# Kernel tuning notes

Hardware: AMD Instinct MI355X
Metric: run time of the kernel (lower is better)

## Reference

```python
import jax, jax.numpy as jnp
import numpy as np

B, T, C = 2, 4096, 768
H = 12
D = C // H  # head_dim = 64
SCALE = np.sqrt(D).astype(np.float32)


def setup_inputs() -> dict:
    key = jax.random.key(0)
    ks = jax.random.split(key, 5)
    s = 0.02
    return {
        "x": jax.random.normal(ks[0], (B, T, C), dtype=jnp.float32),
        "Wqkv": jax.random.normal(ks[1], (C, 3 * C), dtype=jnp.float32) * s,
        "bqkv": jnp.zeros((3 * C,), dtype=jnp.float32),
        "Wout": jax.random.normal(ks[2], (C, C), dtype=jnp.float32) * s,
        "bout": jnp.zeros((C,), dtype=jnp.float32),
    }


def reference(x, Wqkv, bqkv, Wout, bout):
    Bx, Tx, Cx = x.shape
    qkv = x @ Wqkv + bqkv                                   # [B,T,3C]
    qkv = qkv.reshape(Bx, Tx, 3, H, D)
    q, k, v = [jnp.moveaxis(qkv[:, :, i], 2, 1) for i in range(3)]  # each [B,H,T,D]
    attn = jnp.einsum("bhqd,bhkd->bhqk", q, k) / SCALE      # [B,H,T,T]
    causal = jnp.tril(jnp.ones((Tx, Tx), dtype=bool))
    attn = jnp.where(causal, attn, jnp.float32(-jnp.inf))
    attn = jax.nn.softmax(attn, axis=-1)
    out = jnp.einsum("bhqk,bhkd->bhqd", attn, v)            # [B,H,T,D]
    out = jnp.moveaxis(out, 1, 2).reshape(Bx, Tx, Cx)       # [B,T,C]
    return out @ Wout + bout
```

## Files before the change

kernel.cpp:

```cpp
#include <hip/hip_runtime.h>
#include <hip/hip_bf16.h>

#define T_DIM 4096
#define H_N 12
#define D_H 64
#define C_DIM 768
#define B_N 2

typedef short bf16x8 __attribute__((ext_vector_type(8)));
typedef float f32x4 __attribute__((ext_vector_type(4)));
typedef float f32x16 __attribute__((ext_vector_type(16)));

__device__ __forceinline__ short f2bf(float f) {
    union { float f; unsigned u; } x; x.f = f;
    unsigned r = x.u + 0x7fffu + ((x.u >> 16) & 1u);
    return (short)(r >> 16);
}
__device__ __forceinline__ unsigned pk2bf(float a, float b) {
    union { float f; unsigned u; } x, y; x.f = a; y.f = b;
    unsigned ua = x.u + 0x7fffu + ((x.u >> 16) & 1u);
    unsigned ub = y.u + 0x7fffu + ((y.u >> 16) & 1u);
    return (ua >> 16) | (ub & 0xffff0000u);
}
__device__ __forceinline__ unsigned pktrunc(float lo, float hi) {
    union { float f; unsigned u; } a, b; a.f = lo; b.f = hi;
    return __builtin_amdgcn_perm(b.u, a.u, 0x07060302u);
}
__device__ __forceinline__ float bf2f(short s) {
    union { unsigned u; float f; } x; x.u = ((unsigned)(unsigned short)s) << 16;
    return x.f;
}

__device__ __forceinline__ void async_copy16(const void* g, void* l) {
    __builtin_amdgcn_global_load_lds(
        (const __attribute__((address_space(1))) unsigned*)g,
        (__attribute__((address_space(3))) unsigned*)l, 16, 0, 0);
}

#define Q_SCALE 0.18033688011112042f

__global__ __launch_bounds__(256) void xconv_kernel(
    const float* __restrict__ x, short* __restrict__ xb)
{
    size_t i = ((size_t)blockIdx.x * 256 + threadIdx.x) * 8;
    float4 a = *(const float4*)(x + i);
    float4 b = *(const float4*)(x + i + 4);
    unsigned pk[4];
    pk[0] = pk2bf(a.x, a.y); pk[1] = pk2bf(a.z, a.w);
    pk[2] = pk2bf(b.x, b.y); pk[3] = pk2bf(b.z, b.w);
    *(uint4*)(xb + i) = *(uint4*)pk;
}

__global__ __launch_bounds__(256) void wtrans_kernel(
    const float* __restrict__ W, short* __restrict__ Wt, int K, int N)
{
    const int wave = threadIdx.x >> 6, lane = threadIdx.x & 63;
    const int n = blockIdx.x * 256 + wave * 64 + lane;
    const int k0 = blockIdx.y * 128;
    for (int k = k0; k < k0 + 128; k += 8) {
        unsigned pk[4];
#pragma unroll
        for (int j = 0; j < 4; ++j)
            pk[j] = pk2bf(W[(size_t)(k + 2 * j) * N + n],
                          W[(size_t)(k + 2 * j + 1) * N + n]);
        *(uint4*)(Wt + (size_t)n * K + k) = *(uint4*)pk;
    }
}

__global__ __launch_bounds__(256) void qkv_kernel(
    const short* __restrict__ xb, const short* __restrict__ Wb,
    const float* __restrict__ bias,
    short* __restrict__ Qo, short* __restrict__ Ko, short* __restrict__ Vto)
{
    __shared__ short As[128 * 32];
    __shared__ short Bs[128 * 32];
    __shared__ short Vs[64][136];

    const int tid  = threadIdx.x;
    const int wave = tid >> 6, lane = tid & 63;
    const int quad = lane >> 4, l16 = lane & 15;
    const int wm = wave >> 1, wn = wave & 1;
    const int m0 = blockIdx.y * 128, n0 = blockIdx.x * 128;
    const int lrow = lane >> 2, lcc = lane & 3;

    f32x4 acc[4][4];
#pragma unroll
    for (int i = 0; i < 4; ++i)
#pragma unroll
        for (int j = 0; j < 4; ++j) acc[i][j] = (f32x4){0.f, 0.f, 0.f, 0.f};

    for (int k0 = 0; k0 < 768; k0 += 32) {
        __syncthreads();
#pragma unroll
        for (int i = 0; i < 2; ++i) {
            const int sbase = wave * 128 + i * 64;
            const int row = wave * 32 + i * 16 + lrow;
            async_copy16(xb + (size_t)(m0 + row) * 768 + k0 + lcc * 8, &As[sbase * 8]);
            async_copy16(Wb + (size_t)(n0 + row) * 768 + k0 + lcc * 8, &Bs[sbase * 8]);
        }
        asm volatile("s_waitcnt vmcnt(0)" ::: "memory");
        __syncthreads();

        bf16x8 af[4], bfr[4];
#pragma unroll
        for (int t = 0; t < 4; ++t)
            af[t] = *(const bf16x8*)&As[(wm * 64 + t * 16 + l16) * 32 + quad * 8];
#pragma unroll
        for (int t = 0; t < 4; ++t)
            bfr[t] = *(const bf16x8*)&Bs[(wn * 64 + t * 16 + l16) * 32 + quad * 8];
#pragma unroll
        for (int mt = 0; mt < 4; ++mt)
#pragma unroll
            for (int nt = 0; nt < 4; ++nt)
                acc[mt][nt] = __builtin_amdgcn_mfma_f32_16x16x32_bf16(
                    af[mt], bfr[nt], acc[mt][nt], 0, 0, 0);
    }

    if (n0 < 1536) {
#pragma unroll
        for (int nt = 0; nt < 4; ++nt) {
            int n = n0 + wn * 64 + nt * 16 + l16;
            float bv = bias[n];
            int which = n >= 768;
            int cw = n - which * 768;
            int h = cw >> 6, d = cw & 63;
            float scale = which ? 1.0f : Q_SCALE;
            short* dst = which ? Ko : Qo;
#pragma unroll
            for (int mt = 0; mt < 4; ++mt) {
#pragma unroll
                for (int reg = 0; reg < 4; ++reg) {
                    int m = m0 + wm * 64 + mt * 16 + quad * 4 + reg;
                    int b = m >> 12, t = m & 4095;
                    dst[(size_t)((b * H_N + h) * T_DIM + t) * D_H + d] =
                        f2bf((acc[mt][nt][reg] + bv) * scale);
                }
            }
        }
    } else {
        const int b = m0 >> 12, t0 = m0 & 4095;
        for (int p = 0; p < 2; ++p) {
            if (wn == p) {
#pragma unroll
                for (int nt = 0; nt < 4; ++nt) {
                    int n = n0 + wn * 64 + nt * 16 + l16;
                    float bv = bias[n];
#pragma unroll
                    for (int mt = 0; mt < 4; ++mt)
#pragma unroll
                        for (int reg = 0; reg < 4; ++reg)
                            Vs[nt * 16 + l16][wm * 64 + mt * 16 + quad * 4 + reg] =
                                f2bf(acc[mt][nt][reg] + bv);
                }
            }
            __syncthreads();
            int hh = ((n0 - 1536) >> 6) + p;
#pragma unroll
            for (int cc = tid; cc < 512; cc += 256) {
                int d = cc >> 3, part = cc & 7;
                bf16x8 v0 = *(const bf16x8*)&Vs[d][part * 16];
                bf16x8 v1 = *(const bf16x8*)&Vs[d][part * 16 + 8];
                size_t dst = ((size_t)(b * H_N + hh) * D_H + d) * T_DIM + t0 + part * 16;
                *(bf16x8*)(Vto + dst) = v0;
                *(bf16x8*)(Vto + dst + 8) = v1;
            }
            __syncthreads();
        }
    }
}

__global__ __launch_bounds__(256, 4) void attn_partial_kernel(
    const short* __restrict__ Q, const short* __restrict__ K,
    const short* __restrict__ Vt, short* __restrict__ Opart,
    float* __restrict__ Lbuf)
{
    __shared__ short KsT[2][4096];
    __shared__ short VsT[2][4096];

    const int tid  = threadIdx.x;
    const int wave = tid >> 6, lane = tid & 63;
    const int l32 = lane & 31, hi = lane >> 5;
    const int bh = blockIdx.y;
    const int rr = blockIdx.x;

    int qj, ci;
    if (rr < 12) { qj = 12 + rr; ci = 0; }
    else if (rr < 28) { int t = rr - 12; qj = 24 + (t >> 1); ci = t & 1; }
    else {
        int t = rr - 28;
        if (t < 8) { int g = t >> 1, b = t & 1; int m = 12 - g;
                     qj = b ? (11 + m) : (m - 1); }
        else { int tt = t - 8; int g = tt / 3, b = tt - 3 * g; int m = 8 - g;
               qj = (b == 0) ? (m - 1) : ((b == 1) ? (11 + m) : (23 + m)); }
        ci = qj / 12;
    }
    const int q0 = qj * 128;
    const int kvStart = ci * 1536;
    const int kvEnd = min(kvStart + 1536, q0 + 128);
    const int ntiles = (kvEnd - kvStart) >> 6;
    const int off = (qj < 12) ? qj : ((qj < 24) ? 12 + (qj - 12) * 2
                                               : 36 + (qj - 24) * 3);
    const int s = bh * 60 + off + ci;
    const size_t base = (size_t)bh * T_DIM * D_H;
    const int row0 = q0 + wave * 32;
    const int qrow = row0 + l32;

    bf16x8 qf[4];
#pragma unroll
    for (int dk = 0; dk < 4; ++dk)
        qf[dk] = *(const bf16x8*)(
            Q + base + (size_t)(row0 + l32) * 64 + dk * 16 + hi * 8);

    bf16x8 ones;
#pragma unroll
    for (int j = 0; j < 8; ++j) ones[j] = (short)0x3F80;

    f32x16 oacc[2], lacc;
#pragma unroll
    for (int r = 0; r < 16; ++r) { oacc[0][r] = 0.f; oacc[1][r] = 0.f; lacc[r] = 0.f; }

    const int srow = (wave * 128 + lane) >> 3;
    const int scol0 = (lane & 7) ^ (srow & 7);
    const int srow1 = (wave * 128 + 64 + lane) >> 3;
    const int scol1 = (lane & 7) ^ (srow1 & 7);

    {
        const int kv0 = kvStart;
        async_copy16(K + base + (size_t)(kv0 + srow) * 64 + scol0 * 8,
                     &KsT[0][(wave * 128) * 8]);
        async_copy16(Vt + base + (size_t)srow * T_DIM + kv0 + scol0 * 8,
                     &VsT[0][(wave * 128) * 8]);
        async_copy16(K + base + (size_t)(kv0 + srow1) * 64 + scol1 * 8,
                     &KsT[0][(wave * 128 + 64) * 8]);
        async_copy16(Vt + base + (size_t)srow1 * T_DIM + kv0 + scol1 * 8,
                     &VsT[0][(wave * 128 + 64) * 8]);
    }

    int buf = 0;
    for (int it = 0; it < ntiles; ++it) {
        const int kv0 = kvStart + it * 64;

        asm volatile("s_waitcnt vmcnt(0)" ::: "memory");
        asm volatile("s_barrier" ::: "memory");

        if (it + 1 < ntiles) {
            const int kn = kv0 + 64;
            async_copy16(K + base + (size_t)(kn + srow) * 64 + scol0 * 8,
                         &KsT[buf ^ 1][(wave * 128) * 8]);
            async_copy16(Vt + base + (size_t)srow * T_DIM + kn + scol0 * 8,
                         &VsT[buf ^ 1][(wave * 128) * 8]);
            async_copy16(K + base + (size_t)(kn + srow1) * 64 + scol1 * 8,
                         &KsT[buf ^ 1][(wave * 128 + 64) * 8]);
            async_copy16(Vt + base + (size_t)srow1 * T_DIM + kn + scol1 * 8,
                         &VsT[buf ^ 1][(wave * 128 + 64) * 8]);
        }

        if (kv0 <= row0 + 31) {
            const short* Kb = &KsT[buf][0];
            const short* Vb = &VsT[buf][0];

#pragma unroll
            for (int sub = 0; sub < 2; ++sub) {
                if (kv0 + sub * 32 > row0 + 31) continue;

                f32x16 sacc;
#pragma unroll
                for (int r = 0; r < 16; ++r) sacc[r] = 0.f;
#pragma unroll
                for (int dk = 0; dk < 4; ++dk) {
                    int R = sub * 32 + l32;
                    bf16x8 kf = *(const bf16x8*)
                        &Kb[(R * 8 + ((dk * 2 + hi) ^ (R & 7))) * 8];
                    sacc = __builtin_amdgcn_mfma_f32_32x32x16_bf16(
                        kf, qf[dk], sacc, 0, 0, 0);
                }

                if (kv0 + sub * 32 + 31 > row0) {
#pragma unroll
                    for (int r = 0; r < 16; ++r) {
                        int kvg = kv0 + sub * 32 + (r & 3) + 8 * (r >> 2) + 4 * hi;
                        if (kvg > qrow) sacc[r] = -1e30f;
                    }
                }

                unsigned w[8];
#pragma unroll
                for (int r2 = 0; r2 < 8; ++r2)
                    w[r2] = pktrunc(exp2f(sacc[2 * r2]), exp2f(sacc[2 * r2 + 1]));

                asm volatile("v_permlane32_swap_b32 %0, %1" : "+v"(w[0]), "+v"(w[2]));
                asm volatile("v_permlane32_swap_b32 %0, %1" : "+v"(w[1]), "+v"(w[3]));
                asm volatile("v_permlane32_swap_b32 %0, %1" : "+v"(w[4]), "+v"(w[6]));
                asm volatile("v_permlane32_swap_b32 %0, %1" : "+v"(w[5]), "+v"(w[7]));
                union { unsigned u[4]; bf16x8 v; } af0, af1;
                af0.u[0] = w[0]; af0.u[1] = w[1]; af0.u[2] = w[2]; af0.u[3] = w[3];
                af1.u[0] = w[4]; af1.u[1] = w[5]; af1.u[2] = w[6]; af1.u[3] = w[7];

                lacc = __builtin_amdgcn_mfma_f32_32x32x16_bf16(
                    af0.v, ones, lacc, 0, 0, 0);
                lacc = __builtin_amdgcn_mfma_f32_32x32x16_bf16(
                    af1.v, ones, lacc, 0, 0, 0);

#pragma unroll
                for (int kh = 0; kh < 2; ++kh) {
                    bf16x8 pa = kh ? af1.v : af0.v;
#pragma unroll
                    for (int dt = 0; dt < 2; ++dt) {
                        int R = dt * 32 + l32;
                        bf16x8 vf = *(const bf16x8*)
                            &Vb[(R * 8 + ((sub * 4 + kh * 2 + hi) ^ (R & 7))) * 8];
                        oacc[dt] = __builtin_amdgcn_mfma_f32_32x32x16_bf16(
                            pa, vf, oacc[dt], 0, 0, 0);
                    }
                }
            }
        }
        buf ^= 1;
    }

    short* op = Opart + (size_t)s * 8192;
#pragma unroll
    for (int dt = 0; dt < 2; ++dt)
#pragma unroll
        for (int r = 0; r < 16; ++r) {
            int qr = wave * 32 + (r & 3) + 8 * (r >> 2) + 4 * hi;
            op[qr * 64 + dt * 32 + l32] = f2bf(oacc[dt][r]);
        }
    if (l32 == 0) {
#pragma unroll
        for (int r = 0; r < 16; ++r)
            Lbuf[s * 128 + wave * 32 + (r & 3) + 8 * (r >> 2) + 4 * hi] = lacc[r];
    }
}

__global__ __launch_bounds__(256) void combine_kernel(
    const short* __restrict__ Opart, const float* __restrict__ Lbuf,
    short* __restrict__ O)
{
    const int tid = threadIdx.x;
    const int qi = blockIdx.x, bh = blockIdx.y;
    const int b = bh / H_N, h = bh - b * H_N;
    const int r = tid >> 2, cg = (tid & 3) * 16;
    const int qj = qi >> 1;
    const int riu = (qi & 1) * 64 + r;
    const int off = (qj < 12) ? qj : ((qj < 24) ? 12 + (qj - 12) * 2
                                               : 36 + (qj - 24) * 3);
    const int nc = qj / 12 + 1;
    const int s0 = bh * 60 + off;

    float l = 0.f;
    float res[16];
#pragma unroll
    for (int j = 0; j < 16; ++j) res[j] = 0.f;

    for (int ci = 0; ci < nc; ++ci) {
        const int su = s0 + ci;
        l += Lbuf[su * 128 + riu];
        const short* p = Opart + (size_t)su * 8192 + riu * 64 + cg;
        bf16x8 a0 = *(const bf16x8*)p;
        bf16x8 a1 = *(const bf16x8*)(p + 8);
#pragma unroll
        for (int j = 0; j < 8; ++j) { res[j] += bf2f(a0[j]); res[8 + j] += bf2f(a1[j]); }
    }

    float inv = 1.0f / l;
    unsigned pk[8];
#pragma unroll
    for (int j = 0; j < 8; ++j) pk[j] = pk2bf(res[2 * j] * inv, res[2 * j + 1] * inv);
    size_t o = ((size_t)b * T_DIM + qi * 64 + r) * C_DIM + h * 64 + cg;
    *(uint4*)(O + o)     = *(uint4*)&pk[0];
    *(uint4*)(O + o + 8) = *(uint4*)&pk[4];
}

__global__ __launch_bounds__(256) void out_kernel(
    const short* __restrict__ A, const short* __restrict__ Wb,
    const float* __restrict__ bias, float* __restrict__ out)
{
    __shared__ short As[128 * 32];
    __shared__ short Bs[128 * 32];

    const int tid  = threadIdx.x;
    const int wave = tid >> 6, lane = tid & 63;
    const int quad = lane >> 4, l16 = lane & 15;
    const int wm = wave >> 1, wn = wave & 1;
    const int m0 = blockIdx.y * 128, n0 = blockIdx.x * 128;
    const int lrow = lane >> 2, lcc = lane & 3;

    f32x4 acc[4][4];
#pragma unroll
    for (int i = 0; i < 4; ++i)
#pragma unroll
        for (int j = 0; j < 4; ++j) acc[i][j] = (f32x4){0.f, 0.f, 0.f, 0.f};

    for (int k0 = 0; k0 < 768; k0 += 32) {
        __syncthreads();
#pragma unroll
        for (int i = 0; i < 2; ++i) {
            const int sbase = wave * 128 + i * 64;
            const int row = wave * 32 + i * 16 + lrow;
            async_copy16(A  + (size_t)(m0 + row) * 768 + k0 + lcc * 8, &As[sbase * 8]);
            async_copy16(Wb + (size_t)(n0 + row) * 768 + k0 + lcc * 8, &Bs[sbase * 8]);
        }
        asm volatile("s_waitcnt vmcnt(0)" ::: "memory");
        __syncthreads();

        bf16x8 af[4], bfr[4];
#pragma unroll
        for (int t = 0; t < 4; ++t)
            af[t] = *(const bf16x8*)&As[(wm * 64 + t * 16 + l16) * 32 + quad * 8];
#pragma unroll
        for (int t = 0; t < 4; ++t)
            bfr[t] = *(const bf16x8*)&Bs[(wn * 64 + t * 16 + l16) * 32 + quad * 8];
#pragma unroll
        for (int mt = 0; mt < 4; ++mt)
#pragma unroll
            for (int nt = 0; nt < 4; ++nt)
                acc[mt][nt] = __builtin_amdgcn_mfma_f32_16x16x32_bf16(
                    af[mt], bfr[nt], acc[mt][nt], 0, 0, 0);
    }

#pragma unroll
    for (int nt = 0; nt < 4; ++nt) {
        int n = n0 + wn * 64 + nt * 16 + l16;
        float bv = bias[n];
#pragma unroll
        for (int mt = 0; mt < 4; ++mt) {
#pragma unroll
            for (int reg = 0; reg < 4; ++reg) {
                int m = m0 + wm * 64 + mt * 16 + quad * 4 + reg;
                out[(size_t)m * 768 + n] = acc[mt][nt][reg] + bv;
            }
        }
    }
}

extern "C" void kernel_launch(void* const* d_in, const int* in_sizes, int n_in,
                              void* d_out, int out_size, void* d_ws, size_t ws_size,
                              hipStream_t stream) {
    const float* x    = (const float*)d_in[0];
    const float* Wqkv = (const float*)d_in[1];
    const float* bqkv = (const float*)d_in[2];
    const float* Wout = (const float*)d_in[3];
    const float* bout = (const float*)d_in[4];
    float* out = (float*)d_out;

    const size_t per = (size_t)B_N * H_N * T_DIM * D_H;
    short* Q      = (short*)d_ws;
    short* K      = Q + per;
    short* Vt     = K + per;
    short* Woutb  = Vt + per;
    short* xb     = Woutb + (size_t)768 * 768;
    short* Wqkvb  = xb + per;
    short* Opart  = xb;
    float* Lbuf   = (float*)(Opart + (size_t)1440 * 8192);
    short* O      = Q;

    xconv_kernel<<<dim3(3072), 256, 0, stream>>>(x, xb);
    wtrans_kernel<<<dim3(9, 6), 256, 0, stream>>>(Wqkv, Wqkvb, 768, 2304);
    wtrans_kernel<<<dim3(3, 6), 256, 0, stream>>>(Wout, Woutb, 768, 768);
    qkv_kernel<<<dim3(18, 64), 256, 0, stream>>>(xb, Wqkvb, bqkv, Q, K, Vt);
    attn_partial_kernel<<<dim3(60, 24), 256, 0, stream>>>(Q, K, Vt, Opart, Lbuf);
    combine_kernel<<<dim3(64, 24), 256, 0, stream>>>(Opart, Lbuf, O);
    out_kernel<<<dim3(6, 64), 256, 0, stream>>>(O, Woutb, bout, out);
}
```

Before: 308.9 us.

## Rebalance split-KV attention into smaller chunks, fuse prep kernels, add mask-free tile path

Merges the x conversion and the two weight-transpose kernels into one prep launch to save launch overhead. The KV chunk for split attention shrinks from 1536 to 1152, giving 74 work units per head instead of 60 with a rebalanced schedule, so the causal workload spreads more evenly across CUs. The tile body moves into a templated helper with a mask-free fast path for fully unmasked tiles, and s_setprio hints are placed around the MFMA sections. More partials raise combine traffic and workspace use slightly.

```diff
diff --git a/kernel.cpp b/kernel.cpp
--- a/kernel.cpp
+++ b/kernel.cpp
@@ -39,24 +39,17 @@
 
 #define Q_SCALE 0.18033688011112042f
 
-__global__ __launch_bounds__(256) void xconv_kernel(
-    const float* __restrict__ x, short* __restrict__ xb)
-{
-    size_t i = ((size_t)blockIdx.x * 256 + threadIdx.x) * 8;
-    float4 a = *(const float4*)(x + i);
-    float4 b = *(const float4*)(x + i + 4);
-    unsigned pk[4];
-    pk[0] = pk2bf(a.x, a.y); pk[1] = pk2bf(a.z, a.w);
-    pk[2] = pk2bf(b.x, b.y); pk[3] = pk2bf(b.z, b.w);
-    *(uint4*)(xb + i) = *(uint4*)pk;
-}
-
-__global__ __launch_bounds__(256) void wtrans_kernel(
-    const float* __restrict__ W, short* __restrict__ Wt, int K, int N)
-{
-    const int wave = threadIdx.x >> 6, lane = threadIdx.x & 63;
-    const int n = blockIdx.x * 256 + wave * 64 + lane;
-    const int k0 = blockIdx.y * 128;
+#define CHUNK 1152
+#define UNITS_PB 74
+#define SLOTS_PB 74
+
+__device__ __forceinline__ void wtrans_body(
+    const float* __restrict__ W, short* __restrict__ Wt, int K, int N,
+    int bx, int by, int tid)
+{
+    const int wave = tid >> 6, lane = tid & 63;
+    const int n = bx * 256 + wave * 64 + lane;
+    const int k0 = by * 128;
     for (int k = k0; k < k0 + 128; k += 8) {
         unsigned pk[4];
 #pragma unroll
@@ -64,6 +57,30 @@
             pk[j] = pk2bf(W[(size_t)(k + 2 * j) * N + n],
                           W[(size_t)(k + 2 * j + 1) * N + n]);
         *(uint4*)(Wt + (size_t)n * K + k) = *(uint4*)pk;
+    }
+}
+
+__global__ __launch_bounds__(256) void prep_kernel(
+    const float* __restrict__ x, short* __restrict__ xb,
+    const float* __restrict__ Wqkv, short* __restrict__ Wqkvb,
+    const float* __restrict__ Wout, short* __restrict__ Woutb)
+{
+    const int bid = blockIdx.x;
+    const int tid = threadIdx.x;
+    if (bid < 3072) {
+        size_t i = ((size_t)bid * 256 + tid) * 8;
+        float4 a = *(const float4*)(x + i);
+        float4 b = *(const float4*)(x + i + 4);
+        unsigned pk[4];
+        pk[0] = pk2bf(a.x, a.y); pk[1] = pk2bf(a.z, a.w);
+        pk[2] = pk2bf(b.x, b.y); pk[3] = pk2bf(b.z, b.w);
+        *(uint4*)(xb + i) = *(uint4*)pk;
+    } else if (bid < 3126) {
+        int u = bid - 3072;
+        wtrans_body(Wqkv, Wqkvb, 768, 2304, u % 9, u / 9, tid);
+    } else {
+        int u = bid - 3126;
+        wtrans_body(Wout, Woutb, 768, 768, u % 3, u / 3, tid);
     }
 }
 
@@ -169,6 +186,71 @@
     }
 }
 
+template<bool EDGE>
+__device__ __forceinline__ void attn_tile(
+    const short* __restrict__ Kb, const short* __restrict__ Vb,
+    const bf16x8 (&qf)[4], const bf16x8& ones,
+    f32x16& oacc0, f32x16& oacc1, f32x16& lacc,
+    int kv0, int row0, int l32, int hi, int qrow)
+{
+#pragma unroll
+    for (int sub = 0; sub < 2; ++sub) {
+        if (EDGE && (kv0 + sub * 32 > row0 + 31)) continue;
+
+        f32x16 sacc;
+#pragma unroll
+        for (int r = 0; r < 16; ++r) sacc[r] = 0.f;
+        const int R = sub * 32 + l32;
+        __builtin_amdgcn_s_setprio(1);
+#pragma unroll
+        for (int dk = 0; dk < 4; ++dk) {
+            bf16x8 kf = *(const bf16x8*)
+                &Kb[(R * 8 + ((dk * 2 + hi) ^ (R & 7))) * 8];
+            sacc = __builtin_amdgcn_mfma_f32_32x32x16_bf16(kf, qf[dk], sacc, 0, 0, 0);
+        }
+        __builtin_amdgcn_s_setprio(0);
+
+        if (EDGE && (kv0 + sub * 32 + 31 > row0)) {
+#pragma unroll
+            for (int r = 0; r < 16; ++r) {
+                int kvg = kv0 + sub * 32 + (r & 3) + 8 * (r >> 2) + 4 * hi;
+                if (kvg > qrow) sacc[r] = -1e30f;
+            }
+        }
+
+        unsigned w[8];
+#pragma unroll
+        for (int r2 = 0; r2 < 8; ++r2)
+            w[r2] = pktrunc(exp2f(sacc[2 * r2]), exp2f(sacc[2 * r2 + 1]));
+
+        asm volatile("v_permlane32_swap_b32 %0, %1" : "+v"(w[0]), "+v"(w[2]));
+        asm volatile("v_permlane32_swap_b32 %0, %1" : "+v"(w[1]), "+v"(w[3]));
+        asm volatile("v_permlane32_swap_b32 %0, %1" : "+v"(w[4]), "+v"(w[6]));
+        asm volatile("v_permlane32_swap_b32 %0, %1" : "+v"(w[5]), "+v"(w[7]));
+        union { unsigned u[4]; bf16x8 v; } af0, af1;
+        af0.u[0] = w[0]; af0.u[1] = w[1]; af0.u[2] = w[2]; af0.u[3] = w[3];
+        af1.u[0] = w[4]; af1.u[1] = w[5]; af1.u[2] = w[6]; af1.u[3] = w[7];
+
+        __builtin_amdgcn_s_setprio(1);
+        lacc = __builtin_amdgcn_mfma_f32_32x32x16_bf16(af0.v, ones, lacc, 0, 0, 0);
+        lacc = __builtin_amdgcn_mfma_f32_32x32x16_bf16(af1.v, ones, lacc, 0, 0, 0);
+
+#pragma unroll
+        for (int kh = 0; kh < 2; ++kh) {
+            bf16x8 pa = kh ? af1.v : af0.v;
+#pragma unroll
+            for (int dt = 0; dt < 2; ++dt) {
+                int Rv = dt * 32 + l32;
+                bf16x8 vf = *(const bf16x8*)
+                    &Vb[(Rv * 8 + ((sub * 4 + kh * 2 + hi) ^ (Rv & 7))) * 8];
+                f32x16& oa = dt ? oacc1 : oacc0;
+                oa = __builtin_amdgcn_mfma_f32_32x32x16_bf16(pa, vf, oa, 0, 0, 0);
+            }
+        }
+        __builtin_amdgcn_s_setprio(0);
+    }
+}
+
 __global__ __launch_bounds__(256, 4) void attn_partial_kernel(
     const short* __restrict__ Q, const short* __restrict__ K,
     const short* __restrict__ Vt, short* __restrict__ Opart,
@@ -184,27 +266,29 @@
     const int rr = blockIdx.x;
 
     int qj, ci;
-    if (rr < 12) { qj = 12 + rr; ci = 0; }
-    else if (rr < 28) { int t = rr - 12; qj = 24 + (t >> 1); ci = t & 1; }
-    else {
-        int t = rr - 28;
-        if (t < 8) { int g = t >> 1, b = t & 1; int m = 12 - g;
-                     qj = b ? (11 + m) : (m - 1); }
-        else { int tt = t - 8; int g = tt / 3, b = tt - 3 * g; int m = 8 - g;
-               qj = (b == 0) ? (m - 1) : ((b == 1) ? (11 + m) : (23 + m)); }
-        ci = qj / 12;
-    }
+    if (rr < 9)       { qj = 9 + rr; ci = 0; }
+    else if (rr < 27) { int u = rr - 9;  qj = 18 + (u >> 1); ci = u & 1; }
+    else if (rr < 42) { int u = rr - 27; qj = 27 + u / 3; ci = u % 3; }
+    else if (rr < 54) { int t = rr - 42; int m = 8 - t / 3; int idx = t % 3;
+                        qj = m + 9 * idx; ci = idx; }
+    else              { int t = rr - 54; int m = 4 - (t >> 2); int idx = t & 3;
+                        qj = m + 9 * idx; ci = idx; }
+
     const int q0 = qj * 128;
-    const int kvStart = ci * 1536;
-    const int kvEnd = min(kvStart + 1536, q0 + 128);
+    const int kvStart = ci * CHUNK;
+    const int kvEnd = min(kvStart + CHUNK, q0 + 128);
     const int ntiles = (kvEnd - kvStart) >> 6;
-    const int off = (qj < 12) ? qj : ((qj < 24) ? 12 + (qj - 12) * 2
-                                               : 36 + (qj - 24) * 3);
-    const int s = bh * 60 + off + ci;
+    const int off = (qj < 9)  ? qj
+                  : (qj < 18) ? 9 + (qj - 9) * 2
+                  : (qj < 27) ? 27 + (qj - 18) * 3
+                              : 54 + (qj - 27) * 4;
+    const int s = bh * SLOTS_PB + off + ci;
     const size_t base = (size_t)bh * T_DIM * D_H;
     const int row0 = q0 + wave * 32;
     const int qrow = row0 + l32;
 
+    const int nfull = min(ntiles, max(0, (row0 - kvStart + 1) >> 6));
+
     bf16x8 qf[4];
 #pragma unroll
     for (int dk = 0; dk < 4; ++dk)
@@ -215,9 +299,9 @@
 #pragma unroll
     for (int j = 0; j < 8; ++j) ones[j] = (short)0x3F80;
 
-    f32x16 oacc[2], lacc;
-#pragma unroll
-    for (int r = 0; r < 16; ++r) { oacc[0][r] = 0.f; oacc[1][r] = 0.f; lacc[r] = 0.f; }
+    f32x16 oacc0, oacc1, lacc;
+#pragma unroll
+    for (int r = 0; r < 16; ++r) { oacc0[r] = 0.f; oacc1[r] = 0.f; lacc[r] = 0.f; }
 
     const int srow = (wave * 128 + lane) >> 3;
     const int scol0 = (lane & 7) ^ (srow & 7);
@@ -255,77 +339,23 @@
                          &VsT[buf ^ 1][(wave * 128 + 64) * 8]);
         }
 
-        if (kv0 <= row0 + 31) {
-            const short* Kb = &KsT[buf][0];
-            const short* Vb = &VsT[buf][0];
-
-#pragma unroll
-            for (int sub = 0; sub < 2; ++sub) {
-                if (kv0 + sub * 32 > row0 + 31) continue;
-
-                f32x16 sacc;
-#pragma unroll
-                for (int r = 0; r < 16; ++r) sacc[r] = 0.f;
-#pragma unroll
-                for (int dk = 0; dk < 4; ++dk) {
-                    int R = sub * 32 + l32;
-                    bf16x8 kf = *(const bf16x8*)
-                        &Kb[(R * 8 + ((dk * 2 + hi) ^ (R & 7))) * 8];
-                    sacc = __builtin_amdgcn_mfma_f32_32x32x16_bf16(
-                        kf, qf[dk], sacc, 0, 0, 0);
-                }
-
-                if (kv0 + sub * 32 + 31 > row0) {
-#pragma unroll
-                    for (int r = 0; r < 16; ++r) {
-                        int kvg = kv0 + sub * 32 + (r & 3) + 8 * (r >> 2) + 4 * hi;
-                        if (kvg > qrow) sacc[r] = -1e30f;
-                    }
-                }
-
-                unsigned w[8];
-#pragma unroll
-                for (int r2 = 0; r2 < 8; ++r2)
-                    w[r2] = pktrunc(exp2f(sacc[2 * r2]), exp2f(sacc[2 * r2 + 1]));
-
-                asm volatile("v_permlane32_swap_b32 %0, %1" : "+v"(w[0]), "+v"(w[2]));
-                asm volatile("v_permlane32_swap_b32 %0, %1" : "+v"(w[1]), "+v"(w[3]));
-                asm volatile("v_permlane32_swap_b32 %0, %1" : "+v"(w[4]), "+v"(w[6]));
-                asm volatile("v_permlane32_swap_b32 %0, %1" : "+v"(w[5]), "+v"(w[7]));
-                union { unsigned u[4]; bf16x8 v; } af0, af1;
-                af0.u[0] = w[0]; af0.u[1] = w[1]; af0.u[2] = w[2]; af0.u[3] = w[3];
-                af1.u[0] = w[4]; af1.u[1] = w[5]; af1.u[2] = w[6]; af1.u[3] = w[7];
-
-                lacc = __builtin_amdgcn_mfma_f32_32x32x16_bf16(
-                    af0.v, ones, lacc, 0, 0, 0);
-                lacc = __builtin_amdgcn_mfma_f32_32x32x16_bf16(
-                    af1.v, ones, lacc, 0, 0, 0);
-
-#pragma unroll
-                for (int kh = 0; kh < 2; ++kh) {
-                    bf16x8 pa = kh ? af1.v : af0.v;
-#pragma unroll
-                    for (int dt = 0; dt < 2; ++dt) {
-                        int R = dt * 32 + l32;
-                        bf16x8 vf = *(const bf16x8*)
-                            &Vb[(R * 8 + ((sub * 4 + kh * 2 + hi) ^ (R & 7))) * 8];
-                        oacc[dt] = __builtin_amdgcn_mfma_f32_32x32x16_bf16(
-                            pa, vf, oacc[dt], 0, 0, 0);
-                    }
-                }
-            }
+        if (it < nfull) {
+            attn_tile<false>(&KsT[buf][0], &VsT[buf][0], qf, ones,
+                             oacc0, oacc1, lacc, kv0, row0, l32, hi, qrow);
+        } else if (kv0 <= row0 + 31) {
+            attn_tile<true>(&KsT[buf][0], &VsT[buf][0], qf, ones,
+                            oacc0, oacc1, lacc, kv0, row0, l32, hi, qrow);
         }
         buf ^= 1;
     }
 
     short* op = Opart + (size_t)s * 8192;
 #pragma unroll
-    for (int dt = 0; dt < 2; ++dt)
-#pragma unroll
-        for (int r = 0; r < 16; ++r) {
-            int qr = wave * 32 + (r & 3) + 8 * (r >> 2) + 4 * hi;
-            op[qr * 64 + dt * 32 + l32] = f2bf(oacc[dt][r]);
-        }
+    for (int r = 0; r < 16; ++r) {
+        int qr = wave * 32 + (r & 3) + 8 * (r >> 2) + 4 * hi;
+        op[qr * 64 + l32]      = f2bf(oacc0[r]);
+        op[qr * 64 + 32 + l32] = f2bf(oacc1[r]);
+    }
     if (l32 == 0) {
 #pragma unroll
         for (int r = 0; r < 16; ++r)
@@ -343,10 +373,12 @@
     const int r = tid >> 2, cg = (tid & 3) * 16;
     const int qj = qi >> 1;
     const int riu = (qi & 1) * 64 + r;
-    const int off = (qj < 12) ? qj : ((qj < 24) ? 12 + (qj - 12) * 2
-                                               : 36 + (qj - 24) * 3);
-    const int nc = qj / 12 + 1;
-    const int s0 = bh * 60 + off;
+    const int off = (qj < 9)  ? qj
+                  : (qj < 18) ? 9 + (qj - 9) * 2
+                  : (qj < 27) ? 27 + (qj - 18) * 3
+                              : 54 + (qj - 27) * 4;
+    const int nc = qj / 9 + 1;
+    const int s0 = bh * SLOTS_PB + off;
 
     float l = 0.f;
     float res[16];
@@ -452,14 +484,12 @@
     short* xb     = Woutb + (size_t)768 * 768;
     short* Wqkvb  = xb + per;
     short* Opart  = xb;
-    float* Lbuf   = (float*)(Opart + (size_t)1440 * 8192);
+    float* Lbuf   = (float*)(Opart + (size_t)24 * SLOTS_PB * 8192);
     short* O      = Q;
 
-    xconv_kernel<<<dim3(3072), 256, 0, stream>>>(x, xb);
-    wtrans_kernel<<<dim3(9, 6), 256, 0, stream>>>(Wqkv, Wqkvb, 768, 2304);
-    wtrans_kernel<<<dim3(3, 6), 256, 0, stream>>>(Wout, Woutb, 768, 768);
+    prep_kernel<<<dim3(3144), 256, 0, stream>>>(x, xb, Wqkv, Wqkvb, Wout, Woutb);
     qkv_kernel<<<dim3(18, 64), 256, 0, stream>>>(xb, Wqkvb, bqkv, Q, K, Vt);
-    attn_partial_kernel<<<dim3(60, 24), 256, 0, stream>>>(Q, K, Vt, Opart, Lbuf);
+    attn_partial_kernel<<<dim3(UNITS_PB, 24), 256, 0, stream>>>(Q, K, Vt, Opart, Lbuf);
     combine_kernel<<<dim3(64, 24), 256, 0, stream>>>(Opart, Lbuf, O);
     out_kernel<<<dim3(6, 64), 256, 0, stream>>>(O, Woutb, bout, out);
 }
```

Measured after the change: 294.1 us. 1.05x faster.
